# Kernel tuning notes

Measured on AMD Instinct MI355X. Metric: run time of the kernel, lower is better.

## Reference

```python
import jax, jax.numpy as jnp
import numpy as np

B, IN, H, OUT = 32, 128, 1024, 128  # batch, input(charset), hidden, output(charset)


def setup_inputs() -> dict:
    key = jax.random.key(0)
    ks = jax.random.split(key, 10)
    scale = 0.02  # small fast-weight init (candidate_weights start at zero and accumulate)
    d = {}
    d["x"] = jax.random.normal(ks[0], (B, IN), jnp.float32)
    d["hidden"] = jax.random.normal(ks[1], (B, H), jnp.float32)
    # Per-sample dynamic (fast) weight matrices: candidate_weights of each HebbianLinear,
    # shape [batch_size, out_features, in_features] as in the torch module.
    d["W0"] = jax.random.normal(ks[2], (B, H, IN + H), jnp.float32) * scale  # layer 0: (in+hid)->hid
    d["b0"] = jnp.zeros((H,), jnp.float32)
    d["W1"] = jax.random.normal(ks[3], (B, H, H), jnp.float32) * scale      # layer 1
    d["b1"] = jnp.zeros((H,), jnp.float32)
    d["W2"] = jax.random.normal(ks[4], (B, H, H), jnp.float32) * scale      # layer 2
    d["b2"] = jnp.zeros((H,), jnp.float32)
    d["Wh"] = jax.random.normal(ks[5], (B, H, H), jnp.float32) * scale      # i2h head
    d["bh"] = jnp.zeros((H,), jnp.float32)
    d["Wo"] = jax.random.normal(ks[6], (B, OUT, H), jnp.float32) * scale    # i2o head (is_last_layer)
    d["bo"] = jnp.zeros((OUT,), jnp.float32)
    return d


def _hebbian_linear(W, b, x):
    # torch: torch.bmm(candidate_weights, input.unsqueeze(2)).squeeze(2) + bias
    return jnp.einsum('boi,bi->bo', W, x) + b


def reference(x, hidden, W0, b0, W1, b1, W2, b2, Wh, bh, Wo, bo):
    # combined = cat(input, hidden); stack of HebbianLinear layers with tanh nonlinearity
    combined = jnp.concatenate([x, hidden], axis=1)          # [B, IN+H]
    combined = jnp.tanh(_hebbian_linear(W0, b0, combined))   # [B, H]
    combined = jnp.tanh(_hebbian_linear(W1, b1, combined))
    combined = jnp.tanh(_hebbian_linear(W2, b2, combined))
    # dropout is identity in eval mode
    new_hidden = jnp.tanh(_hebbian_linear(Wh, bh, combined))  # [B, H]
    logits = _hebbian_linear(Wo, bo, combined)                # [B, OUT]
    output = jax.nn.log_softmax(logits, axis=1)
    return output, new_hidden
```

## Files before the change

kernel.cpp:

```cpp
#include <hip/hip_runtime.h>
#include <math.h>


#define B_SZ 32
#define IN_SZ 128
#define H_SZ 1024
#define OUT_SZ 128

typedef float f4 __attribute__((ext_vector_type(4)));

__device__ __forceinline__ float dot4(f4 w, f4 a, float acc) {
    acc = fmaf(w.x, a.x, acc);
    acc = fmaf(w.y, a.y, acc);
    acc = fmaf(w.z, a.z, acc);
    acc = fmaf(w.w, a.w, acc);
    return acc;
}

__device__ __forceinline__ float wave_allreduce(float s) {
    #pragma unroll
    for (int off = 32; off > 0; off >>= 1)
        s += __shfl_xor(s, off, 64);
    return s;
}

__global__ __launch_bounds__(256) void gemv0_kernel(
        const float* __restrict__ W, const float* __restrict__ bias,
        const float* __restrict__ x, const float* __restrict__ h,
        float* __restrict__ out) {
    int wave = blockIdx.x * 4 + (threadIdx.x >> 6);
    int lane = threadIdx.x & 63;
    int r0 = wave << 2;
    int b = r0 >> 10;

    const f4* __restrict__ x4 = (const f4*)(x + b * IN_SZ);
    const f4* __restrict__ h4 = (const f4*)(h + b * H_SZ);

    f4 a[4];
    #pragma unroll
    for (int k = 0; k < 4; k++) {
        int j = lane + 64 * k;
        a[k] = (j < 32) ? x4[j] : h4[j - 32];
    }
    f4 a4;
    if (lane < 32) a4 = h4[224 + lane];

    float s0 = 0.f, s1 = 0.f, s2 = 0.f, s3 = 0.f;
    #pragma unroll
    for (int r = 0; r < 4; r++) {
        const f4* __restrict__ Wr = (const f4*)(W + (size_t)(r0 + r) * (IN_SZ + H_SZ));
        float s = 0.f;
        #pragma unroll
        for (int k = 0; k < 4; k++)
            s = dot4(__builtin_nontemporal_load(Wr + lane + 64 * k), a[k], s);
        if (lane < 32)
            s = dot4(__builtin_nontemporal_load(Wr + 256 + lane), a4, s);
        if      (r == 0) s0 = s;
        else if (r == 1) s1 = s;
        else if (r == 2) s2 = s;
        else             s3 = s;
    }
    s0 = wave_allreduce(s0);
    s1 = wave_allreduce(s1);
    s2 = wave_allreduce(s2);
    s3 = wave_allreduce(s3);
    if (lane < 4) {
        float v = (lane == 0) ? s0 : (lane == 1) ? s1 : (lane == 2) ? s2 : s3;
        int o = (r0 & (H_SZ - 1)) + lane;
        out[r0 + lane] = tanhf(v + bias[o]);
    }
}

__global__ __launch_bounds__(256) void gemv_mid_kernel(
        const float* __restrict__ W, const float* __restrict__ bias,
        const float* __restrict__ v, float* __restrict__ out) {
    int wave = blockIdx.x * 4 + (threadIdx.x >> 6);
    int lane = threadIdx.x & 63;
    int r0 = wave << 2;
    int b = r0 >> 10;

    const f4* __restrict__ vr = (const f4*)(v + b * H_SZ);
    f4 a[4];
    #pragma unroll
    for (int k = 0; k < 4; k++) a[k] = vr[lane + 64 * k];

    float s0 = 0.f, s1 = 0.f, s2 = 0.f, s3 = 0.f;
    #pragma unroll
    for (int r = 0; r < 4; r++) {
        const f4* __restrict__ Wr = (const f4*)(W + (size_t)(r0 + r) * H_SZ);
        float s = 0.f;
        #pragma unroll
        for (int k = 0; k < 4; k++)
            s = dot4(__builtin_nontemporal_load(Wr + lane + 64 * k), a[k], s);
        if      (r == 0) s0 = s;
        else if (r == 1) s1 = s;
        else if (r == 2) s2 = s;
        else             s3 = s;
    }
    s0 = wave_allreduce(s0);
    s1 = wave_allreduce(s1);
    s2 = wave_allreduce(s2);
    s3 = wave_allreduce(s3);
    if (lane < 4) {
        float v2 = (lane == 0) ? s0 : (lane == 1) ? s1 : (lane == 2) ? s2 : s3;
        int o = (r0 & (H_SZ - 1)) + lane;
        out[r0 + lane] = tanhf(v2 + bias[o]);
    }
}

__global__ __launch_bounds__(256) void heads_kernel(
        const float* __restrict__ Wh, const float* __restrict__ bh,
        const float* __restrict__ Wo, const float* __restrict__ bo,
        const float* __restrict__ v,
        float* __restrict__ new_hidden, float* __restrict__ logits) {
    int wave = blockIdx.x * 4 + (threadIdx.x >> 6);
    int lane = threadIdx.x & 63;
    int r0 = wave << 2;
    bool isO = r0 >= B_SZ * H_SZ;
    int rr = isO ? r0 - B_SZ * H_SZ : r0;
    int b = isO ? (rr >> 7) : (rr >> 10);

    const float* Wbase = isO ? (Wo + (size_t)rr * H_SZ) : (Wh + (size_t)rr * H_SZ);
    const f4* __restrict__ vr = (const f4*)(v + b * H_SZ);
    f4 a[4];
    #pragma unroll
    for (int k = 0; k < 4; k++) a[k] = vr[lane + 64 * k];

    float s0 = 0.f, s1 = 0.f, s2 = 0.f, s3 = 0.f;
    #pragma unroll
    for (int r = 0; r < 4; r++) {
        const f4* __restrict__ Wr = (const f4*)(Wbase + (size_t)r * H_SZ);
        float s = 0.f;
        #pragma unroll
        for (int k = 0; k < 4; k++)
            s = dot4(__builtin_nontemporal_load(Wr + lane + 64 * k), a[k], s);
        if      (r == 0) s0 = s;
        else if (r == 1) s1 = s;
        else if (r == 2) s2 = s;
        else             s3 = s;
    }
    s0 = wave_allreduce(s0);
    s1 = wave_allreduce(s1);
    s2 = wave_allreduce(s2);
    s3 = wave_allreduce(s3);
    if (lane < 4) {
        float s = (lane == 0) ? s0 : (lane == 1) ? s1 : (lane == 2) ? s2 : s3;
        if (isO) {
            int o = (rr & (OUT_SZ - 1)) + lane;
            logits[rr + lane] = s + bo[o];
        } else {
            int o = (rr & (H_SZ - 1)) + lane;
            new_hidden[rr + lane] = tanhf(s + bh[o]);
        }
    }
}

__global__ void logsoftmax_kernel(const float* __restrict__ logits,
                                  float* __restrict__ out) {
    int b = blockIdx.x;
    int lane = threadIdx.x;
    float v0 = logits[b * OUT_SZ + lane];
    float v1 = logits[b * OUT_SZ + 64 + lane];
    float m = fmaxf(v0, v1);
    #pragma unroll
    for (int off = 32; off > 0; off >>= 1)
        m = fmaxf(m, __shfl_xor(m, off, 64));
    float e = __expf(v0 - m) + __expf(v1 - m);
    #pragma unroll
    for (int off = 32; off > 0; off >>= 1)
        e += __shfl_xor(e, off, 64);
    float lse = m + logf(e);
    out[b * OUT_SZ + lane]      = v0 - lse;
    out[b * OUT_SZ + 64 + lane] = v1 - lse;
}

extern "C" void kernel_launch(void* const* d_in, const int* in_sizes, int n_in,
                              void* d_out, int out_size, void* d_ws, size_t ws_size,
                              hipStream_t stream) {
    const float* x      = (const float*)d_in[0];
    const float* hidden = (const float*)d_in[1];
    const float* W0 = (const float*)d_in[2];
    const float* b0 = (const float*)d_in[3];
    const float* W1 = (const float*)d_in[4];
    const float* b1 = (const float*)d_in[5];
    const float* W2 = (const float*)d_in[6];
    const float* b2 = (const float*)d_in[7];
    const float* Wh = (const float*)d_in[8];
    const float* bh = (const float*)d_in[9];
    const float* Wo = (const float*)d_in[10];
    const float* bo = (const float*)d_in[11];

    float* out_ls     = (float*)d_out;
    float* new_hidden = out_ls + B_SZ * OUT_SZ;

    float* ws = (float*)d_ws;
    float* c1 = ws;
    float* c2 = c1 + B_SZ * H_SZ;
    float* logits = c2 + B_SZ * H_SZ;

    const int blocksH = (B_SZ * H_SZ) / 16;
    gemv0_kernel<<<blocksH, 256, 0, stream>>>(W0, b0, x, hidden, c1);
    gemv_mid_kernel<<<blocksH, 256, 0, stream>>>(W1, b1, c1, c2);
    gemv_mid_kernel<<<blocksH, 256, 0, stream>>>(W2, b2, c2, c1);

    const int blocksHeads = (B_SZ * H_SZ + B_SZ * OUT_SZ) / 16;
    heads_kernel<<<blocksHeads, 256, 0, stream>>>(Wh, bh, Wo, bo, c1, new_hidden, logits);

    logsoftmax_kernel<<<B_SZ, 64, 0, stream>>>(logits, out_ls);
}
```

Baseline: 453.7 us.

## Fuse all GEMV layers into one persistent kernel with grid barriers

Replaces the five separate launches (three hidden GEMVs, heads, log-softmax) with a single kernel of 1024 blocks that steps through the stages, separated by atomic-counter grid barriers in workspace that is zeroed by a memset. Each wave now handles 8 rows instead of 4, the head stage folds the Wo row into the same wave, and the nontemporal weight loads become plain loads. The goal is to remove launch gaps and stage tails between dependent kernels. The cost is the spin barriers and a requirement that all 1024 blocks be co-resident (launch bounds of 4 blocks per CU); otherwise the kernel can deadlock.

```diff
diff --git a/kernel.cpp b/kernel.cpp
--- a/kernel.cpp
+++ b/kernel.cpp
@@ -6,6 +6,7 @@
 #define IN_SZ 128
 #define H_SZ 1024
 #define OUT_SZ 128
+#define NBLOCK 1024
 
 typedef float f4 __attribute__((ext_vector_type(4)));
 
@@ -24,154 +25,162 @@
     return s;
 }
 
-__global__ __launch_bounds__(256) void gemv0_kernel(
-        const float* __restrict__ W, const float* __restrict__ bias,
-        const float* __restrict__ x, const float* __restrict__ h,
-        float* __restrict__ out) {
-    int wave = blockIdx.x * 4 + (threadIdx.x >> 6);
-    int lane = threadIdx.x & 63;
-    int r0 = wave << 2;
-    int b = r0 >> 10;
-
-    const f4* __restrict__ x4 = (const f4*)(x + b * IN_SZ);
-    const f4* __restrict__ h4 = (const f4*)(h + b * H_SZ);
-
+__device__ __forceinline__ float sel8(const float acc[8], int lane) {
+    float v = acc[0];
+    v = (lane == 1) ? acc[1] : v;
+    v = (lane == 2) ? acc[2] : v;
+    v = (lane == 3) ? acc[3] : v;
+    v = (lane == 4) ? acc[4] : v;
+    v = (lane == 5) ? acc[5] : v;
+    v = (lane == 6) ? acc[6] : v;
+    v = (lane == 7) ? acc[7] : v;
+    return v;
+}
+
+__device__ __forceinline__ void grid_barrier(unsigned* __restrict__ bar, int idx) {
+    __syncthreads();
+    if (threadIdx.x == 0) {
+        __threadfence();
+        atomicAdd(&bar[idx], 1u);
+        while (__hip_atomic_load(&bar[idx], __ATOMIC_ACQUIRE,
+                                 __HIP_MEMORY_SCOPE_AGENT) < (unsigned)NBLOCK) {
+            __builtin_amdgcn_s_sleep(1);
+        }
+    }
+    __syncthreads();
+    __threadfence();
+}
+
+__device__ __forceinline__ void mid8(const float* __restrict__ W,
+                                     const float* __restrict__ bias,
+                                     const float* __restrict__ vin,
+                                     float* __restrict__ vout,
+                                     int w, int lane) {
+    int r0 = w << 3;
+    int b  = w >> 7;
+    const f4* __restrict__ vr = (const f4*)(vin + b * H_SZ);
     f4 a[4];
     #pragma unroll
-    for (int k = 0; k < 4; k++) {
-        int j = lane + 64 * k;
-        a[k] = (j < 32) ? x4[j] : h4[j - 32];
-    }
-    f4 a4;
-    if (lane < 32) a4 = h4[224 + lane];
-
-    float s0 = 0.f, s1 = 0.f, s2 = 0.f, s3 = 0.f;
-    #pragma unroll
-    for (int r = 0; r < 4; r++) {
-        const f4* __restrict__ Wr = (const f4*)(W + (size_t)(r0 + r) * (IN_SZ + H_SZ));
-        float s = 0.f;
-        #pragma unroll
-        for (int k = 0; k < 4; k++)
-            s = dot4(__builtin_nontemporal_load(Wr + lane + 64 * k), a[k], s);
-        if (lane < 32)
-            s = dot4(__builtin_nontemporal_load(Wr + 256 + lane), a4, s);
-        if      (r == 0) s0 = s;
-        else if (r == 1) s1 = s;
-        else if (r == 2) s2 = s;
-        else             s3 = s;
-    }
-    s0 = wave_allreduce(s0);
-    s1 = wave_allreduce(s1);
-    s2 = wave_allreduce(s2);
-    s3 = wave_allreduce(s3);
-    if (lane < 4) {
-        float v = (lane == 0) ? s0 : (lane == 1) ? s1 : (lane == 2) ? s2 : s3;
-        int o = (r0 & (H_SZ - 1)) + lane;
-        out[r0 + lane] = tanhf(v + bias[o]);
-    }
-}
-
-__global__ __launch_bounds__(256) void gemv_mid_kernel(
-        const float* __restrict__ W, const float* __restrict__ bias,
-        const float* __restrict__ v, float* __restrict__ out) {
-    int wave = blockIdx.x * 4 + (threadIdx.x >> 6);
-    int lane = threadIdx.x & 63;
-    int r0 = wave << 2;
-    int b = r0 >> 10;
-
-    const f4* __restrict__ vr = (const f4*)(v + b * H_SZ);
-    f4 a[4];
-    #pragma unroll
     for (int k = 0; k < 4; k++) a[k] = vr[lane + 64 * k];
 
-    float s0 = 0.f, s1 = 0.f, s2 = 0.f, s3 = 0.f;
-    #pragma unroll
-    for (int r = 0; r < 4; r++) {
+    float acc[8];
+    #pragma unroll
+    for (int r = 0; r < 8; r++) {
         const f4* __restrict__ Wr = (const f4*)(W + (size_t)(r0 + r) * H_SZ);
         float s = 0.f;
         #pragma unroll
-        for (int k = 0; k < 4; k++)
-            s = dot4(__builtin_nontemporal_load(Wr + lane + 64 * k), a[k], s);
-        if      (r == 0) s0 = s;
-        else if (r == 1) s1 = s;
-        else if (r == 2) s2 = s;
-        else             s3 = s;
-    }
-    s0 = wave_allreduce(s0);
-    s1 = wave_allreduce(s1);
-    s2 = wave_allreduce(s2);
-    s3 = wave_allreduce(s3);
-    if (lane < 4) {
-        float v2 = (lane == 0) ? s0 : (lane == 1) ? s1 : (lane == 2) ? s2 : s3;
-        int o = (r0 & (H_SZ - 1)) + lane;
-        out[r0 + lane] = tanhf(v2 + bias[o]);
-    }
-}
-
-__global__ __launch_bounds__(256) void heads_kernel(
+        for (int k = 0; k < 4; k++) s = dot4(Wr[lane + 64 * k], a[k], s);
+        acc[r] = s;
+    }
+    #pragma unroll
+    for (int r = 0; r < 8; r++) acc[r] = wave_allreduce(acc[r]);
+    if (lane < 8) {
+        float s = sel8(acc, lane);
+        vout[r0 + lane] = tanhf(s + bias[(r0 & (H_SZ - 1)) + lane]);
+    }
+}
+
+__global__ __launch_bounds__(256, 4) void fused_kernel(
+        const float* __restrict__ x, const float* __restrict__ hidden,
+        const float* __restrict__ W0, const float* __restrict__ b0,
+        const float* __restrict__ W1, const float* __restrict__ b1,
+        const float* __restrict__ W2, const float* __restrict__ b2,
         const float* __restrict__ Wh, const float* __restrict__ bh,
         const float* __restrict__ Wo, const float* __restrict__ bo,
-        const float* __restrict__ v,
-        float* __restrict__ new_hidden, float* __restrict__ logits) {
-    int wave = blockIdx.x * 4 + (threadIdx.x >> 6);
-    int lane = threadIdx.x & 63;
-    int r0 = wave << 2;
-    bool isO = r0 >= B_SZ * H_SZ;
-    int rr = isO ? r0 - B_SZ * H_SZ : r0;
-    int b = isO ? (rr >> 7) : (rr >> 10);
-
-    const float* Wbase = isO ? (Wo + (size_t)rr * H_SZ) : (Wh + (size_t)rr * H_SZ);
-    const f4* __restrict__ vr = (const f4*)(v + b * H_SZ);
-    f4 a[4];
-    #pragma unroll
-    for (int k = 0; k < 4; k++) a[k] = vr[lane + 64 * k];
-
-    float s0 = 0.f, s1 = 0.f, s2 = 0.f, s3 = 0.f;
-    #pragma unroll
-    for (int r = 0; r < 4; r++) {
-        const f4* __restrict__ Wr = (const f4*)(Wbase + (size_t)r * H_SZ);
-        float s = 0.f;
-        #pragma unroll
-        for (int k = 0; k < 4; k++)
-            s = dot4(__builtin_nontemporal_load(Wr + lane + 64 * k), a[k], s);
-        if      (r == 0) s0 = s;
-        else if (r == 1) s1 = s;
-        else if (r == 2) s2 = s;
-        else             s3 = s;
-    }
-    s0 = wave_allreduce(s0);
-    s1 = wave_allreduce(s1);
-    s2 = wave_allreduce(s2);
-    s3 = wave_allreduce(s3);
-    if (lane < 4) {
-        float s = (lane == 0) ? s0 : (lane == 1) ? s1 : (lane == 2) ? s2 : s3;
-        if (isO) {
-            int o = (rr & (OUT_SZ - 1)) + lane;
-            logits[rr + lane] = s + bo[o];
-        } else {
-            int o = (rr & (H_SZ - 1)) + lane;
-            new_hidden[rr + lane] = tanhf(s + bh[o]);
-        }
-    }
-}
-
-__global__ void logsoftmax_kernel(const float* __restrict__ logits,
-                                  float* __restrict__ out) {
-    int b = blockIdx.x;
-    int lane = threadIdx.x;
-    float v0 = logits[b * OUT_SZ + lane];
-    float v1 = logits[b * OUT_SZ + 64 + lane];
-    float m = fmaxf(v0, v1);
-    #pragma unroll
-    for (int off = 32; off > 0; off >>= 1)
-        m = fmaxf(m, __shfl_xor(m, off, 64));
-    float e = __expf(v0 - m) + __expf(v1 - m);
-    #pragma unroll
-    for (int off = 32; off > 0; off >>= 1)
-        e += __shfl_xor(e, off, 64);
-    float lse = m + logf(e);
-    out[b * OUT_SZ + lane]      = v0 - lse;
-    out[b * OUT_SZ + 64 + lane] = v1 - lse;
+        unsigned* __restrict__ bar,
+        float* __restrict__ c1, float* __restrict__ c2,
+        float* __restrict__ logits, float* __restrict__ out_ls,
+        float* __restrict__ new_hidden) {
+    const int w    = blockIdx.x * 4 + (threadIdx.x >> 6);
+    const int lane = threadIdx.x & 63;
+    const int r0   = w << 3;
+    const int b    = w >> 7;
+
+    {
+        const f4* __restrict__ x4 = (const f4*)(x + b * IN_SZ);
+        const f4* __restrict__ h4 = (const f4*)(hidden + b * H_SZ);
+        f4 a[4];
+        #pragma unroll
+        for (int k = 0; k < 4; k++) {
+            int j = lane + 64 * k;
+            a[k] = (j < 32) ? x4[j] : h4[j - 32];
+        }
+        f4 a4 = {0.f, 0.f, 0.f, 0.f};
+        if (lane < 32) a4 = h4[224 + lane];
+
+        float acc[8];
+        #pragma unroll
+        for (int r = 0; r < 8; r++) {
+            const f4* __restrict__ Wr = (const f4*)(W0 + (size_t)(r0 + r) * (IN_SZ + H_SZ));
+            float s = 0.f;
+            #pragma unroll
+            for (int k = 0; k < 4; k++) s = dot4(Wr[lane + 64 * k], a[k], s);
+            if (lane < 32) s = dot4(Wr[256 + lane], a4, s);
+            acc[r] = s;
+        }
+        #pragma unroll
+        for (int r = 0; r < 8; r++) acc[r] = wave_allreduce(acc[r]);
+        if (lane < 8) {
+            float s = sel8(acc, lane);
+            c1[r0 + lane] = tanhf(s + b0[(r0 & (H_SZ - 1)) + lane]);
+        }
+    }
+    grid_barrier(bar, 0);
+
+    mid8(W1, b1, c1, c2, w, lane);
+    grid_barrier(bar, 1);
+    mid8(W2, b2, c2, c1, w, lane);
+    grid_barrier(bar, 2);
+
+    {
+        const f4* __restrict__ vr = (const f4*)(c1 + b * H_SZ);
+        f4 a[4];
+        #pragma unroll
+        for (int k = 0; k < 4; k++) a[k] = vr[lane + 64 * k];
+
+        float acc[8];
+        #pragma unroll
+        for (int r = 0; r < 8; r++) {
+            const f4* __restrict__ Wr = (const f4*)(Wh + (size_t)(r0 + r) * H_SZ);
+            float s = 0.f;
+            #pragma unroll
+            for (int k = 0; k < 4; k++) s = dot4(Wr[lane + 64 * k], a[k], s);
+            acc[r] = s;
+        }
+        const f4* __restrict__ Wor = (const f4*)(Wo + (size_t)w * H_SZ);
+        float so = 0.f;
+        #pragma unroll
+        for (int k = 0; k < 4; k++) so = dot4(Wor[lane + 64 * k], a[k], so);
+
+        #pragma unroll
+        for (int r = 0; r < 8; r++) acc[r] = wave_allreduce(acc[r]);
+        so = wave_allreduce(so);
+
+        if (lane < 8) {
+            float s = sel8(acc, lane);
+            new_hidden[r0 + lane] = tanhf(s + bh[(r0 & (H_SZ - 1)) + lane]);
+        }
+        if (lane == 8) {
+            logits[w] = so + bo[w & (OUT_SZ - 1)];
+        }
+    }
+    grid_barrier(bar, 3);
+
+    if (w < B_SZ) {
+        float v0 = logits[w * OUT_SZ + lane];
+        float v1 = logits[w * OUT_SZ + 64 + lane];
+        float m = fmaxf(v0, v1);
+        #pragma unroll
+        for (int off = 32; off > 0; off >>= 1)
+            m = fmaxf(m, __shfl_xor(m, off, 64));
+        float e = __expf(v0 - m) + __expf(v1 - m);
+        #pragma unroll
+        for (int off = 32; off > 0; off >>= 1)
+            e += __shfl_xor(e, off, 64);
+        float lse = m + logf(e);
+        out_ls[w * OUT_SZ + lane]      = v0 - lse;
+        out_ls[w * OUT_SZ + 64 + lane] = v1 - lse;
+    }
 }
 
 extern "C" void kernel_launch(void* const* d_in, const int* in_sizes, int n_in,
@@ -193,18 +202,15 @@
     float* out_ls     = (float*)d_out;
     float* new_hidden = out_ls + B_SZ * OUT_SZ;
 
-    float* ws = (float*)d_ws;
-    float* c1 = ws;
+    float* wsf = (float*)d_ws;
+    unsigned* bar = (unsigned*)wsf;
+    float* c1 = wsf + 64;
     float* c2 = c1 + B_SZ * H_SZ;
     float* logits = c2 + B_SZ * H_SZ;
 
-    const int blocksH = (B_SZ * H_SZ) / 16;
-    gemv0_kernel<<<blocksH, 256, 0, stream>>>(W0, b0, x, hidden, c1);
-    gemv_mid_kernel<<<blocksH, 256, 0, stream>>>(W1, b1, c1, c2);
-    gemv_mid_kernel<<<blocksH, 256, 0, stream>>>(W2, b2, c2, c1);
-
-    const int blocksHeads = (B_SZ * H_SZ + B_SZ * OUT_SZ) / 16;
-    heads_kernel<<<blocksHeads, 256, 0, stream>>>(Wh, bh, Wo, bo, c1, new_hidden, logits);
-
-    logsoftmax_kernel<<<B_SZ, 64, 0, stream>>>(logits, out_ls);
-}
+    hipMemsetAsync(d_ws, 0, 64, stream);
+
+    fused_kernel<<<NBLOCK, 256, 0, stream>>>(
+        x, hidden, W0, b0, W1, b1, W2, b2, Wh, bh, Wo, bo,
+        bar, c1, c2, logits, out_ls, new_hidden);
+}
```

Measured after the change: 1.295 ms. 2.85x slower.
